# Kernel tuning notes

Measured on AMD Instinct MI355X. Metric: run time of the kernel, lower is better.

## Reference

```python
import jax, jax.numpy as jnp
import numpy as np

B, N, H, HID, MLP = 512, 96, 8, 256, 256
NODE_DIM, EDGE_DIM, E = 32, 7, 196608
DH = HID // H
NEG = -1e9  # stand-in for -inf to keep softmax NaN-free under fp16/bf16


def setup_inputs() -> dict:
    key = jax.random.key(0)
    ks = jax.random.split(key, 24)
    node_features = jax.random.normal(ks[0], (B * N, NODE_DIM), dtype=jnp.float32)
    node_batch = jnp.repeat(jnp.arange(B), N)  # sorted, exactly N nodes per graph
    g = jax.random.randint(ks[1], (E,), 0, B)
    s = jax.random.randint(ks[2], (E,), 0, N)
    d = jax.random.randint(ks[3], (E,), 0, N)
    edge_index = jnp.stack([g * N + s, g * N + d])  # [2, E] global node ids
    edge_attr = jax.random.uniform(ks[4], (E, EDGE_DIM), dtype=jnp.float32)
    def w(k, shape):
        fan_in = shape[0]
        return jax.random.normal(k, shape, dtype=jnp.float32) / np.sqrt(fan_in)
    return {
        "node_features": node_features,
        "edge_attr": edge_attr,
        "W_in1": w(ks[5], (NODE_DIM, MLP)), "b_in1": jnp.zeros((MLP,)),
        "W_in2": w(ks[6], (MLP, HID)), "b_in2": jnp.zeros((HID,)),
        "W_bond": w(ks[7], (EDGE_DIM, H)), "b_bond": jnp.zeros((H,)),
        "Wq": w(ks[8], (HID, HID)), "Wk": w(ks[9], (HID, HID)),
        "Wv": w(ks[10], (HID, HID)), "Wo": w(ks[11], (HID, HID)),
        "W_out1": w(ks[12], (HID, MLP)), "b_out1": jnp.zeros((MLP,)),
        "W_out2": w(ks[13], (MLP, 1)), "b_out2": jnp.zeros((1,)),
        "edge_index": edge_index,
        "node_batch": node_batch,
    }


def reference(node_features, edge_attr, W_in1, b_in1, W_in2, b_in2, W_bond, b_bond,
              Wq, Wk, Wv, Wo, W_out1, b_out1, W_out2, b_out2, edge_index, node_batch):
    # input MLP
    h = jax.nn.relu(node_features @ W_in1 + b_in1) @ W_in2 + b_in2  # [T, HID]
    T = h.shape[0]
    # per-graph node counts and offsets (to_dense_batch)
    counts = jax.ops.segment_sum(jnp.ones((T,), jnp.int32), node_batch, num_segments=B)
    offsets = jnp.concatenate([jnp.zeros((1,), jnp.int32), jnp.cumsum(counts)[:-1]])
    local = jnp.arange(T) - offsets[node_batch]
    dense_h = jnp.zeros((B, N, HID), h.dtype).at[node_batch, local].set(h)
    pad_mask = jnp.arange(N)[None, :] < counts[:, None]  # [B, N]
    # scatter edge features into dense bond bias + adjacency
    src, dst = edge_index
    eb = node_batch[src]
    ls = src - offsets[eb]
    ld = dst - offsets[node_batch[dst]]
    bias_flat = edge_attr @ W_bond + b_bond  # [E, H]
    bond_bias = jnp.zeros((B, N, N, H), bias_flat.dtype).at[eb, ls, ld].set(bias_flat)
    bond_bias = jnp.transpose(bond_bias, (0, 3, 1, 2))  # [B, H, N, N]
    adj = jnp.zeros((B, N, N), bool).at[eb, ls, ld].set(True)
    adj = adj | jnp.eye(N, dtype=bool)[None]  # self-loops so softmax rows are valid
    combined = jnp.where(adj[:, None], bond_bias, NEG)
    combined = jnp.where(pad_mask[:, None, None, :], combined, NEG)
    # masked multi-head attention (ESA)
    q = (dense_h @ Wq).reshape(B, N, H, DH)
    k = (dense_h @ Wk).reshape(B, N, H, DH)
    v = (dense_h @ Wv).reshape(B, N, H, DH)
    scores = jnp.einsum('bqhd,bkhd->bhqk', q, k) / np.sqrt(DH) + combined
    attn = jax.nn.softmax(scores, axis=-1)
    ctx = jnp.einsum('bhqk,bkhd->bqhd', attn, v).reshape(B, N, HID) @ Wo
    # masked mean pooling over valid nodes -> [B, HID]
    pooled = jnp.sum(ctx * pad_mask[..., None], axis=1) / counts[:, None].astype(ctx.dtype)
    logits = jax.nn.relu(pooled @ W_out1 + b_out1) @ W_out2 + b_out2
    return logits.reshape(-1)  # [B]
```

## Files before the change

kernel.cpp:

```cpp
#include <hip/hip_runtime.h>
#include <hip/hip_bf16.h>
#include <hip/hip_fp16.h>

#define BG   512
#define NN   96
#define NH   8
#define HIDD 256
#define DHD  32
#define NDIM 32
#define EDIM 7
#define NE   196608
#define TT   (BG*NN)
#define CELLS (BG*NN*NN)
#define NEGF (-60000.0f)

typedef short bf16x8 __attribute__((ext_vector_type(8)));
typedef float f32x4  __attribute__((ext_vector_type(4)));

#define MFMA16 __builtin_amdgcn_mfma_f32_16x16x32_bf16

__device__ __forceinline__ short f2bf(float x) {
    __hip_bfloat16 b = __float2bfloat16(x);
    return *reinterpret_cast<short*>(&b);
}
__device__ __forceinline__ float h2f(unsigned short u) {
    __half h = __ushort_as_half(u);
    return __half2float(h);
}

__global__ void init_winner_kernel(int* __restrict__ winner) {
    int idx = blockIdx.x * 256 + threadIdx.x;
    ((int4*)winner)[idx] = make_int4(-1, -1, -1, -1);
}

__global__ void scatter_kernel(const int* __restrict__ ei, int* __restrict__ winner) {
    int e = blockIdx.x * 256 + threadIdx.x;
    if (e >= NE) return;
    int src = ei[e], dst = ei[NE + e];
    int b  = src / NN;
    int ls = src - b * NN;
    int ld = dst % NN;
    atomicMax(&winner[b * NN * NN + ls * NN + ld], e);
}

__global__ void init_bias8_kernel(unsigned short* __restrict__ b8) {
    int idx = blockIdx.x * 256 + threadIdx.x;
    int within = idx % 1152;
    int i = within / 12, j0 = (within % 12) * 8;
    unsigned short negh = __half_as_ushort(__float2half(NEGF));
    unsigned short vals[8];
#pragma unroll
    for (int c = 0; c < 8; ++c) vals[c] = (j0 + c == i) ? (unsigned short)0 : negh;
    *(int4*)(b8 + (size_t)idx * 8) = *(int4*)vals;
}

__global__ void scatter_bias8_kernel(const int* __restrict__ ei,
                                     const int* __restrict__ winner,
                                     const float* __restrict__ ea,
                                     const float* __restrict__ Wb,
                                     const float* __restrict__ bb,
                                     unsigned short* __restrict__ b8) {
    int e = blockIdx.x * 256 + threadIdx.x;
    if (e >= NE) return;
    int src = ei[e], dst = ei[NE + e];
    int b  = src / NN;
    int ls = src - b * NN;
    int ld = dst % NN;
    int cell = b * NN * NN + ls * NN + ld;
    if (winner[cell] != e) return;
    float a[EDIM];
#pragma unroll
    for (int j = 0; j < EDIM; ++j) a[j] = ea[(size_t)e * EDIM + j];
#pragma unroll
    for (int hh = 0; hh < NH; ++hh) {
        float acc = bb[hh];
#pragma unroll
        for (int j = 0; j < EDIM; ++j) acc += a[j] * Wb[j * NH + hh];
        b8[(size_t)hh * CELLS + cell] = __half_as_ushort(__float2half(acc));
    }
}

__global__ void convert_w_kernel(const float* __restrict__ W_in2,
                                 const float* __restrict__ Wq,
                                 const float* __restrict__ Wk,
                                 const float* __restrict__ Wv,
                                 const float* __restrict__ W1,
                                 short* __restrict__ wt) {
    int m = blockIdx.x >> 8;
    int k = blockIdx.x & 255;
    if (m == 4) {
        if (k >= NDIM) return;
        wt[((size_t)(4 * HIDD) + threadIdx.x) * HIDD + k] = f2bf(W1[(size_t)k * HIDD + threadIdx.x]);
        return;
    }
    const float* W = (m == 0) ? W_in2 : (m == 1) ? Wq : (m == 2) ? Wk : Wv;
    float v = W[(size_t)k * HIDD + threadIdx.x];
    wt[((size_t)m * HIDD + threadIdx.x) * HIDD + k] = f2bf(v);
}

__global__ __launch_bounds__(256) void mlp_fused_mfma(const float* __restrict__ X,
                                                      const short* __restrict__ wt,
                                                      const float* __restrict__ b1,
                                                      const float* __restrict__ b2,
                                                      short* __restrict__ hbf) {
    __shared__ short As[64][264];
    __shared__ short Ws[256][40];
    int tid = threadIdx.x;
    int row0 = blockIdx.x * 64;
    int w = tid >> 6, l = tid & 63, lr = l & 15, g = l >> 4;
    {
        const float* xrow = X + (size_t)(row0 + w * 16 + lr) * NDIM + g * 8;
        float4 x0 = *(const float4*)xrow;
        float4 x1 = *(const float4*)(xrow + 4);
        bf16x8 af;
        af[0] = f2bf(x0.x); af[1] = f2bf(x0.y); af[2] = f2bf(x0.z); af[3] = f2bf(x0.w);
        af[4] = f2bf(x1.x); af[5] = f2bf(x1.y); af[6] = f2bf(x1.z); af[7] = f2bf(x1.w);
        const short* w1t = wt + (size_t)4 * HIDD * HIDD;
#pragma unroll
        for (int ct = 0; ct < 16; ++ct) {
            bf16x8 bfr = *(const bf16x8*)(w1t + (size_t)(ct * 16 + lr) * HIDD + g * 8);
            f32x4 acc = (f32x4){0.f, 0.f, 0.f, 0.f};
            acc = MFMA16(af, bfr, acc, 0, 0, 0);
            float bb = b1[ct * 16 + lr];
#pragma unroll
            for (int r = 0; r < 4; ++r)
                As[w * 16 + 4 * g + r][ct * 16 + lr] = f2bf(fmaxf(acc[r] + bb, 0.f));
        }
    }
    f32x4 acc[16];
#pragma unroll
    for (int ct = 0; ct < 16; ++ct) acc[ct] = (f32x4){0.f, 0.f, 0.f, 0.f};
    for (int kt = 0; kt < 8; ++kt) {
        __syncthreads();
#pragma unroll
        for (int c = 0; c < 4; ++c) {
            int q = tid + c * 256;
            int n = q >> 2, kc = (q & 3) * 8;
            *(bf16x8*)&Ws[n][kc] = *(const bf16x8*)(wt + (size_t)n * HIDD + kt * 32 + kc);
        }
        __syncthreads();
        bf16x8 af = *(const bf16x8*)&As[w * 16 + lr][kt * 32 + g * 8];
#pragma unroll
        for (int ct = 0; ct < 16; ++ct) {
            bf16x8 bfr = *(const bf16x8*)&Ws[ct * 16 + lr][g * 8];
            acc[ct] = MFMA16(af, bfr, acc[ct], 0, 0, 0);
        }
    }
#pragma unroll
    for (int ct = 0; ct < 16; ++ct) {
        int col = ct * 16 + lr;
        float bb = b2[col];
#pragma unroll
        for (int r = 0; r < 4; ++r) {
            int row = row0 + w * 16 + 4 * g + r;
            hbf[(size_t)row * HIDD + col] = f2bf(acc[ct][r] + bb);
        }
    }
}

#define WSTRIDE 264
#define WSLAB   (32 * WSTRIDE)
__global__ __launch_bounds__(384, 3) void attn_mfma_kernel(const short* __restrict__ hbf,
                                                           const short* __restrict__ wt,
                                                           const unsigned short* __restrict__ b8,
                                                           float* __restrict__ pooled) {
    __shared__ short WL[3 * WSLAB];
    __shared__ float red[24][32];
    short* Qs  = WL;
    short* Ks  = WL + 3840;
    short* Ps  = WL;
    short* VtL = WL + 22016;
    int bid = blockIdx.x;
    int b = (bid & 7) + 8 * (bid >> 6);
    int hh = (bid >> 3) & 7;
    int tid = threadIdx.x;
    int w = tid >> 6;
    int l = tid & 63, lr = l & 15, g = l >> 4;
#pragma unroll
    for (int it = 0; it < 8; ++it) {
        int c = it * 384 + tid;
        int m = c >> 10, cc = c & 1023;
        int n = cc >> 5, kc = (cc & 31) * 8;
        bf16x8 v = *(const bf16x8*)(wt + ((size_t)((1 + m) * HIDD + hh * DHD + n)) * HIDD + kc);
        *(bf16x8*)&WL[m * WSLAB + n * WSTRIDE + kc] = v;
    }
    const unsigned short* bp = b8 + (size_t)hh * CELLS + b * NN * NN;
    unsigned short bv16[6][4];
#pragma unroll
    for (int jt = 0; jt < 6; ++jt)
#pragma unroll
        for (int r = 0; r < 4; ++r)
            bv16[jt][r] = bp[(w * 16 + 4 * g + r) * NN + jt * 16 + lr];
    const short* hrow = hbf + ((size_t)(b * NN + w * 16 + lr)) * HIDD + g * 8;
    bf16x8 a[8];
#pragma unroll
    for (int ks = 0; ks < 8; ++ks) a[ks] = *(const bf16x8*)(hrow + ks * 32);
    __syncthreads();
    f32x4 qac[2], kac[2], vac[2];
#pragma unroll
    for (int ct = 0; ct < 2; ++ct) {
        qac[ct] = (f32x4){0.f, 0.f, 0.f, 0.f};
        kac[ct] = (f32x4){0.f, 0.f, 0.f, 0.f};
        vac[ct] = (f32x4){0.f, 0.f, 0.f, 0.f};
        int nrow = (ct * 16 + lr) * WSTRIDE + g * 8;
#pragma unroll
        for (int ks = 0; ks < 8; ++ks) {
            qac[ct] = MFMA16(a[ks], *(const bf16x8*)&WL[nrow + ks * 32], qac[ct], 0, 0, 0);
            kac[ct] = MFMA16(a[ks], *(const bf16x8*)&WL[WSLAB + nrow + ks * 32], kac[ct], 0, 0, 0);
            vac[ct] = MFMA16(a[ks], *(const bf16x8*)&WL[2 * WSLAB + nrow + ks * 32], vac[ct], 0, 0, 0);
        }
    }
    __syncthreads();
#pragma unroll
    for (int ct = 0; ct < 2; ++ct)
#pragma unroll
        for (int r = 0; r < 4; ++r) {
            int row = w * 16 + 4 * g + r, col = ct * 16 + lr;
            Qs[row * 40 + col]   = f2bf(qac[ct][r]);
            Ks[row * 40 + col]   = f2bf(kac[ct][r]);
            VtL[col * 104 + row] = f2bf(vac[ct][r]);
        }
    __syncthreads();
    float sc[6][4];
    {
        bf16x8 qa = *(const bf16x8*)&Qs[(w * 16 + lr) * 40 + g * 8];
        const float scale = 0.17677669529663687f;
#pragma unroll
        for (int jt = 0; jt < 6; ++jt) {
            bf16x8 kb = *(const bf16x8*)&Ks[(jt * 16 + lr) * 40 + g * 8];
            f32x4 z = (f32x4){0.f, 0.f, 0.f, 0.f};
            f32x4 s = MFMA16(qa, kb, z, 0, 0, 0);
#pragma unroll
            for (int r = 0; r < 4; ++r)
                sc[jt][r] = s[r] * scale + h2f(bv16[jt][r]);
        }
    }
#pragma unroll
    for (int r = 0; r < 4; ++r) {
        float m = sc[0][r];
#pragma unroll
        for (int jt = 1; jt < 6; ++jt) m = fmaxf(m, sc[jt][r]);
        m = fmaxf(m, __shfl_xor(m, 1)); m = fmaxf(m, __shfl_xor(m, 2));
        m = fmaxf(m, __shfl_xor(m, 4)); m = fmaxf(m, __shfl_xor(m, 8));
        float sum = 0.f;
#pragma unroll
        for (int jt = 0; jt < 6; ++jt) { sc[jt][r] = __expf(sc[jt][r] - m); sum += sc[jt][r]; }
        sum += __shfl_xor(sum, 1); sum += __shfl_xor(sum, 2);
        sum += __shfl_xor(sum, 4); sum += __shfl_xor(sum, 8);
        float inv = 1.f / sum;
#pragma unroll
        for (int jt = 0; jt < 6; ++jt) sc[jt][r] *= inv;
    }
    __syncthreads();
#pragma unroll
    for (int r = 0; r < 4; ++r) {
        int i = w * 16 + 4 * g + r;
#pragma unroll
        for (int jt = 0; jt < 6; ++jt)
            Ps[i * 104 + jt * 16 + lr] = f2bf(sc[jt][r]);
    }
    f32x4 c0 = (f32x4){0.f, 0.f, 0.f, 0.f}, c1 = (f32x4){0.f, 0.f, 0.f, 0.f};
#pragma unroll
    for (int kt = 0; kt < 3; ++kt) {
        bf16x8 pa = *(const bf16x8*)&Ps[(w * 16 + lr) * 104 + kt * 32 + g * 8];
        c0 = MFMA16(pa, *(const bf16x8*)&VtL[lr * 104 + kt * 32 + g * 8], c0, 0, 0, 0);
        c1 = MFMA16(pa, *(const bf16x8*)&VtL[(16 + lr) * 104 + kt * 32 + g * 8], c1, 0, 0, 0);
    }
    red[w * 4 + g][lr]      = c0[0] + c0[1] + c0[2] + c0[3];
    red[w * 4 + g][16 + lr] = c1[0] + c1[1] + c1[2] + c1[3];
    __syncthreads();
    if (tid < DHD) {
        float sum = 0.f;
#pragma unroll
        for (int q = 0; q < 24; ++q) sum += red[q][tid];
        pooled[(size_t)b * HIDD + hh * DHD + tid] = sum * (1.f / 96.f);
    }
}

__global__ __launch_bounds__(256) void head_kernel(const float* __restrict__ pooled,
                                                   const float* __restrict__ Wo,
                                                   const float* __restrict__ Wo1,
                                                   const float* __restrict__ bo1,
                                                   const float* __restrict__ Wo2,
                                                   const float* __restrict__ bo2,
                                                   float* __restrict__ out) {
    __shared__ float ps[HIDD];
    __shared__ float ys[HIDD];
    __shared__ float red[4];
    int b = blockIdx.x, tid = threadIdx.x;
    ps[tid] = pooled[(size_t)b * HIDD + tid];
    __syncthreads();
    float acc = 0.f;
    for (int c = 0; c < HIDD; ++c) acc += ps[c] * Wo[c * HIDD + tid];
    ys[tid] = acc;
    __syncthreads();
    float a2 = bo1[tid];
    for (int c = 0; c < HIDD; ++c) a2 += ys[c] * Wo1[c * HIDD + tid];
    float hv = fmaxf(a2, 0.f);
    float p = hv * Wo2[tid];
#pragma unroll
    for (int off = 32; off > 0; off >>= 1) p += __shfl_xor(p, off);
    int lane = tid & 63, wave = tid >> 6;
    if (lane == 0) red[wave] = p;
    __syncthreads();
    if (tid == 0) out[b] = red[0] + red[1] + red[2] + red[3] + bo2[0];
}

extern "C" void kernel_launch(void* const* d_in, const int* in_sizes, int n_in,
                              void* d_out, int out_size, void* d_ws, size_t ws_size,
                              hipStream_t stream) {
    (void)in_sizes; (void)n_in; (void)out_size;
    const float* node_features = (const float*)d_in[0];
    const float* edge_attr     = (const float*)d_in[1];
    const float* W_in1  = (const float*)d_in[2];
    const float* b_in1  = (const float*)d_in[3];
    const float* W_in2  = (const float*)d_in[4];
    const float* b_in2  = (const float*)d_in[5];
    const float* W_bond = (const float*)d_in[6];
    const float* b_bond = (const float*)d_in[7];
    const float* Wq     = (const float*)d_in[8];
    const float* Wk     = (const float*)d_in[9];
    const float* Wv     = (const float*)d_in[10];
    const float* Wo     = (const float*)d_in[11];
    const float* W_out1 = (const float*)d_in[12];
    const float* b_out1 = (const float*)d_in[13];
    const float* W_out2 = (const float*)d_in[14];
    const float* b_out2 = (const float*)d_in[15];
    const int* edge_index = (const int*)d_in[16];
    float* out = (float*)d_out;

    char* ws = (char*)d_ws;
    size_t off = 0;
    auto alloc = [&](size_t bytes) {
        void* p = ws + off;
        off = (off + bytes + 255) & ~(size_t)255;
        return p;
    };
    short*          hbf    = (short*)alloc((size_t)TT * HIDD * 2);
    short*          wt     = (short*)alloc((size_t)5 * HIDD * HIDD * 2);
    unsigned short* b8     = (unsigned short*)alloc((size_t)NH * CELLS * 2);
    int*            winner = (int*)alloc((size_t)CELLS * 4);
    float*          pooled = (float*)alloc((size_t)BG * HIDD * 4);
    if (ws_size < off) return;

    hipLaunchKernelGGL(init_winner_kernel, dim3(CELLS / 1024), dim3(256), 0, stream, winner);
    hipLaunchKernelGGL(scatter_kernel, dim3((NE + 255) / 256), dim3(256), 0, stream, edge_index, winner);
    hipLaunchKernelGGL(init_bias8_kernel, dim3(NH * CELLS / 8 / 256), dim3(256), 0, stream, b8);
    hipLaunchKernelGGL(scatter_bias8_kernel, dim3((NE + 255) / 256), dim3(256), 0, stream,
                       edge_index, winner, edge_attr, W_bond, b_bond, b8);
    hipLaunchKernelGGL(convert_w_kernel, dim3(5 * 256), dim3(256), 0, stream,
                       W_in2, Wq, Wk, Wv, W_in1, wt);
    hipLaunchKernelGGL(mlp_fused_mfma, dim3(TT / 64), dim3(256), 0, stream,
                       node_features, wt, b_in1, b_in2, hbf);
    hipLaunchKernelGGL(attn_mfma_kernel, dim3(BG * NH), dim3(384), 0, stream,
                       hbf, wt, b8, pooled);
    hipLaunchKernelGGL(head_kernel, dim3(BG), dim3(256), 0, stream,
                       pooled, Wo, W_out1, b_out1, W_out2, b_out2, out);
}
```

Measured before the change: 248.5 us.

## Process two graphs per attention block with pre-swizzled QKV weight fragments

The attention kernel now handles two graphs per block for the same head, so each block loads the per-head Q/K/V weight slab once and reuses it for both graphs. The weights are pre-arranged into MFMA fragment order in a new workspace buffer, which lets the kernel copy them into shared memory with flat loads and no padding. The three setup kernels (winner init, bias init, weight convert) are merged into one launch. In exchange, register pressure rises and occupancy drops (launch bounds go from 3 to 2 blocks), and the grid is half as large.

```diff
diff --git a/kernel.cpp b/kernel.cpp
--- a/kernel.cpp
+++ b/kernel.cpp
@@ -28,9 +28,62 @@
     return __half2float(h);
 }
 
-__global__ void init_winner_kernel(int* __restrict__ winner) {
-    int idx = blockIdx.x * 256 + threadIdx.x;
-    ((int4*)winner)[idx] = make_int4(-1, -1, -1, -1);
+#define JA 4608
+#define JB 18432
+#define JC 512
+#define JD 96
+__global__ void setup_kernel(int* __restrict__ winner,
+                             unsigned short* __restrict__ b8,
+                             short* __restrict__ wt,
+                             short* __restrict__ wf,
+                             const float* __restrict__ W_in2,
+                             const float* __restrict__ W1,
+                             const float* __restrict__ Wq,
+                             const float* __restrict__ Wk,
+                             const float* __restrict__ Wv) {
+    int blk = blockIdx.x, tid = threadIdx.x;
+    if (blk < JA) {
+        ((int4*)winner)[blk * 256 + tid] = make_int4(-1, -1, -1, -1);
+        return;
+    }
+    blk -= JA;
+    if (blk < JB) {
+        int idx = blk * 256 + tid;
+        int within = idx % 1152;
+        int i = within / 12, j0 = (within % 12) * 8;
+        unsigned short negh = __half_as_ushort(__float2half(NEGF));
+        unsigned short vals[8];
+#pragma unroll
+        for (int c = 0; c < 8; ++c) vals[c] = (j0 + c == i) ? (unsigned short)0 : negh;
+        *(int4*)(b8 + (size_t)idx * 8) = *(int4*)vals;
+        return;
+    }
+    blk -= JB;
+    if (blk < JC) {
+        int mm = blk >> 8, k = blk & 255;
+        if (mm == 1) {
+            if (k < NDIM)
+                wt[((size_t)(4 * HIDD) + tid) * HIDD + k] = f2bf(W1[(size_t)k * HIDD + tid]);
+        } else {
+            wt[(size_t)tid * HIDD + k] = f2bf(W_in2[(size_t)k * HIDD + tid]);
+        }
+        return;
+    }
+    blk -= JC;
+    {
+        int gi = blk * 4 + (tid >> 6);
+        int lane = tid & 63, lr = lane & 15, gg = lane >> 4;
+        int ks = gi & 7, ct = (gi >> 3) & 1, hh = (gi >> 4) & 7, m = gi >> 7;
+        const float* W = (m == 0) ? Wq : (m == 1) ? Wk : Wv;
+        int col = hh * DHD + ct * 16 + lr;
+        short v[8];
+#pragma unroll
+        for (int e = 0; e < 8; ++e) {
+            int k = ks * 32 + gg * 8 + e;
+            v[e] = f2bf(W[(size_t)k * HIDD + col]);
+        }
+        *(bf16x8*)(wf + ((size_t)gi * 64 + lane) * 8) = *(bf16x8*)v;
+    }
 }
 
 __global__ void scatter_kernel(const int* __restrict__ ei, int* __restrict__ winner) {
@@ -41,17 +94,6 @@
     int ls = src - b * NN;
     int ld = dst % NN;
     atomicMax(&winner[b * NN * NN + ls * NN + ld], e);
-}
-
-__global__ void init_bias8_kernel(unsigned short* __restrict__ b8) {
-    int idx = blockIdx.x * 256 + threadIdx.x;
-    int within = idx % 1152;
-    int i = within / 12, j0 = (within % 12) * 8;
-    unsigned short negh = __half_as_ushort(__float2half(NEGF));
-    unsigned short vals[8];
-#pragma unroll
-    for (int c = 0; c < 8; ++c) vals[c] = (j0 + c == i) ? (unsigned short)0 : negh;
-    *(int4*)(b8 + (size_t)idx * 8) = *(int4*)vals;
 }
 
 __global__ void scatter_bias8_kernel(const int* __restrict__ ei,
@@ -78,24 +120,6 @@
         for (int j = 0; j < EDIM; ++j) acc += a[j] * Wb[j * NH + hh];
         b8[(size_t)hh * CELLS + cell] = __half_as_ushort(__float2half(acc));
     }
-}
-
-__global__ void convert_w_kernel(const float* __restrict__ W_in2,
-                                 const float* __restrict__ Wq,
-                                 const float* __restrict__ Wk,
-                                 const float* __restrict__ Wv,
-                                 const float* __restrict__ W1,
-                                 short* __restrict__ wt) {
-    int m = blockIdx.x >> 8;
-    int k = blockIdx.x & 255;
-    if (m == 4) {
-        if (k >= NDIM) return;
-        wt[((size_t)(4 * HIDD) + threadIdx.x) * HIDD + k] = f2bf(W1[(size_t)k * HIDD + threadIdx.x]);
-        return;
-    }
-    const float* W = (m == 0) ? W_in2 : (m == 1) ? Wq : (m == 2) ? Wk : Wv;
-    float v = W[(size_t)k * HIDD + threadIdx.x];
-    wt[((size_t)m * HIDD + threadIdx.x) * HIDD + k] = f2bf(v);
 }
 
 __global__ __launch_bounds__(256) void mlp_fused_mfma(const float* __restrict__ X,
@@ -158,21 +182,19 @@
     }
 }
 
-#define WSTRIDE 264
-#define WSLAB   (32 * WSTRIDE)
-__global__ __launch_bounds__(384, 3) void attn_mfma_kernel(const short* __restrict__ hbf,
-                                                           const short* __restrict__ wt,
-                                                           const unsigned short* __restrict__ b8,
-                                                           float* __restrict__ pooled) {
-    __shared__ short WL[3 * WSLAB];
-    __shared__ float red[24][32];
-    short* Qs  = WL;
-    short* Ks  = WL + 3840;
-    short* Ps  = WL;
-    short* VtL = WL + 22016;
+__global__ __launch_bounds__(384, 2) void attn2_kernel(const short* __restrict__ hbf,
+                                                       const short* __restrict__ wf,
+                                                       const unsigned short* __restrict__ b8,
+                                                       float* __restrict__ pooled) {
+    __shared__ short WL[24576];
+    __shared__ float red2[2][24][32];
+    short* Qs2 = WL;
+    short* Ks2 = WL + 7680;
+    short* Ps2 = WL;
+    short* Vt2 = WL + 18432;
     int bid = blockIdx.x;
-    int b = (bid & 7) + 8 * (bid >> 6);
-    int hh = (bid >> 3) & 7;
+    int g8 = bid & 7, hh = (bid >> 3) & 7, pr = bid >> 6;
+    int b0 = g8 + 16 * pr, b1 = b0 + 8;
     int tid = threadIdx.x;
     int w = tid >> 6;
     int l = tid & 63, lr = l & 15, g = l >> 4;
@@ -180,34 +202,43 @@
     for (int it = 0; it < 8; ++it) {
         int c = it * 384 + tid;
         int m = c >> 10, cc = c & 1023;
-        int n = cc >> 5, kc = (cc & 31) * 8;
-        bf16x8 v = *(const bf16x8*)(wt + ((size_t)((1 + m) * HIDD + hh * DHD + n)) * HIDD + kc);
-        *(bf16x8*)&WL[m * WSLAB + n * WSTRIDE + kc] = v;
-    }
-    const unsigned short* bp = b8 + (size_t)hh * CELLS + b * NN * NN;
-    unsigned short bv16[6][4];
-#pragma unroll
-    for (int jt = 0; jt < 6; ++jt)
-#pragma unroll
-        for (int r = 0; r < 4; ++r)
-            bv16[jt][r] = bp[(w * 16 + 4 * g + r) * NN + jt * 16 + lr];
-    const short* hrow = hbf + ((size_t)(b * NN + w * 16 + lr)) * HIDD + g * 8;
-    bf16x8 a[8];
-#pragma unroll
-    for (int ks = 0; ks < 8; ++ks) a[ks] = *(const bf16x8*)(hrow + ks * 32);
-    __syncthreads();
-    f32x4 qac[2], kac[2], vac[2];
+        *(bf16x8*)&WL[m * 8192 + cc * 8] =
+            *(const bf16x8*)(wf + (((size_t)(m * 8 + hh)) * 1024 + cc) * 8);
+    }
+    unsigned short bv16[2][6][4];
+#pragma unroll
+    for (int gr = 0; gr < 2; ++gr) {
+        const unsigned short* bp = b8 + (size_t)hh * CELLS + (size_t)(gr ? b1 : b0) * NN * NN;
+#pragma unroll
+        for (int jt = 0; jt < 6; ++jt)
+#pragma unroll
+            for (int r = 0; r < 4; ++r)
+                bv16[gr][jt][r] = bp[(w * 16 + 4 * g + r) * NN + jt * 16 + lr];
+    }
+    const short* h0 = hbf + ((size_t)(b0 * NN + w * 16 + lr)) * HIDD + g * 8;
+    const short* h1 = hbf + ((size_t)(b1 * NN + w * 16 + lr)) * HIDD + g * 8;
+    bf16x8 a0[8], a1[8];
+#pragma unroll
+    for (int ks = 0; ks < 8; ++ks) { a0[ks] = *(const bf16x8*)(h0 + ks * 32);
+                                     a1[ks] = *(const bf16x8*)(h1 + ks * 32); }
+    __syncthreads();
+    f32x4 q0[2], k0[2], v0[2], q1[2], k1[2], v1[2];
 #pragma unroll
     for (int ct = 0; ct < 2; ++ct) {
-        qac[ct] = (f32x4){0.f, 0.f, 0.f, 0.f};
-        kac[ct] = (f32x4){0.f, 0.f, 0.f, 0.f};
-        vac[ct] = (f32x4){0.f, 0.f, 0.f, 0.f};
-        int nrow = (ct * 16 + lr) * WSTRIDE + g * 8;
+        q0[ct] = (f32x4){0.f,0.f,0.f,0.f}; k0[ct] = q0[ct]; v0[ct] = q0[ct];
+        q1[ct] = q0[ct]; k1[ct] = q0[ct]; v1[ct] = q0[ct];
 #pragma unroll
         for (int ks = 0; ks < 8; ++ks) {
-            qac[ct] = MFMA16(a[ks], *(const bf16x8*)&WL[nrow + ks * 32], qac[ct], 0, 0, 0);
-            kac[ct] = MFMA16(a[ks], *(const bf16x8*)&WL[WSLAB + nrow + ks * 32], kac[ct], 0, 0, 0);
-            vac[ct] = MFMA16(a[ks], *(const bf16x8*)&WL[2 * WSLAB + nrow + ks * 32], vac[ct], 0, 0, 0);
+            int fo = ((ct * 8 + ks) * 64 + l) * 8;
+            bf16x8 bq = *(const bf16x8*)&WL[fo];
+            bf16x8 bk = *(const bf16x8*)&WL[8192 + fo];
+            bf16x8 bv = *(const bf16x8*)&WL[16384 + fo];
+            q0[ct] = MFMA16(a0[ks], bq, q0[ct], 0, 0, 0);
+            q1[ct] = MFMA16(a1[ks], bq, q1[ct], 0, 0, 0);
+            k0[ct] = MFMA16(a0[ks], bk, k0[ct], 0, 0, 0);
+            k1[ct] = MFMA16(a1[ks], bk, k1[ct], 0, 0, 0);
+            v0[ct] = MFMA16(a0[ks], bv, v0[ct], 0, 0, 0);
+            v1[ct] = MFMA16(a1[ks], bv, v1[ct], 0, 0, 0);
         }
     }
     __syncthreads();
@@ -216,64 +247,74 @@
 #pragma unroll
         for (int r = 0; r < 4; ++r) {
             int row = w * 16 + 4 * g + r, col = ct * 16 + lr;
-            Qs[row * 40 + col]   = f2bf(qac[ct][r]);
-            Ks[row * 40 + col]   = f2bf(kac[ct][r]);
-            VtL[col * 104 + row] = f2bf(vac[ct][r]);
-        }
-    __syncthreads();
-    float sc[6][4];
-    {
-        bf16x8 qa = *(const bf16x8*)&Qs[(w * 16 + lr) * 40 + g * 8];
-        const float scale = 0.17677669529663687f;
+            Qs2[row * 40 + col]          = f2bf(q0[ct][r]);
+            Qs2[3840 + row * 40 + col]   = f2bf(q1[ct][r]);
+            Ks2[row * 40 + col]          = f2bf(k0[ct][r]);
+            Ks2[3840 + row * 40 + col]   = f2bf(k1[ct][r]);
+            Vt2[col * 96 + row]          = f2bf(v0[ct][r]);
+            Vt2[3072 + col * 96 + row]   = f2bf(v1[ct][r]);
+        }
+    __syncthreads();
+    float sc2[2][6][4];
+    const float scale = 0.17677669529663687f;
+#pragma unroll
+    for (int gr = 0; gr < 2; ++gr) {
+        bf16x8 qa = *(const bf16x8*)&Qs2[gr * 3840 + (w * 16 + lr) * 40 + g * 8];
 #pragma unroll
         for (int jt = 0; jt < 6; ++jt) {
-            bf16x8 kb = *(const bf16x8*)&Ks[(jt * 16 + lr) * 40 + g * 8];
+            bf16x8 kb = *(const bf16x8*)&Ks2[gr * 3840 + (jt * 16 + lr) * 40 + g * 8];
             f32x4 z = (f32x4){0.f, 0.f, 0.f, 0.f};
             f32x4 s = MFMA16(qa, kb, z, 0, 0, 0);
 #pragma unroll
             for (int r = 0; r < 4; ++r)
-                sc[jt][r] = s[r] * scale + h2f(bv16[jt][r]);
-        }
-    }
-#pragma unroll
-    for (int r = 0; r < 4; ++r) {
-        float m = sc[0][r];
-#pragma unroll
-        for (int jt = 1; jt < 6; ++jt) m = fmaxf(m, sc[jt][r]);
-        m = fmaxf(m, __shfl_xor(m, 1)); m = fmaxf(m, __shfl_xor(m, 2));
-        m = fmaxf(m, __shfl_xor(m, 4)); m = fmaxf(m, __shfl_xor(m, 8));
+                sc2[gr][jt][r] = s[r] * scale + h2f(bv16[gr][jt][r]);
+        }
+#pragma unroll
+        for (int r = 0; r < 4; ++r) {
+            float m = sc2[gr][0][r];
+#pragma unroll
+            for (int jt = 1; jt < 6; ++jt) m = fmaxf(m, sc2[gr][jt][r]);
+            m = fmaxf(m, __shfl_xor(m, 1)); m = fmaxf(m, __shfl_xor(m, 2));
+            m = fmaxf(m, __shfl_xor(m, 4)); m = fmaxf(m, __shfl_xor(m, 8));
+            float sum = 0.f;
+#pragma unroll
+            for (int jt = 0; jt < 6; ++jt) { sc2[gr][jt][r] = __expf(sc2[gr][jt][r] - m); sum += sc2[gr][jt][r]; }
+            sum += __shfl_xor(sum, 1); sum += __shfl_xor(sum, 2);
+            sum += __shfl_xor(sum, 4); sum += __shfl_xor(sum, 8);
+            float inv = 1.f / sum;
+#pragma unroll
+            for (int jt = 0; jt < 6; ++jt) sc2[gr][jt][r] *= inv;
+        }
+    }
+    __syncthreads();
+#pragma unroll
+    for (int gr = 0; gr < 2; ++gr)
+#pragma unroll
+        for (int r = 0; r < 4; ++r) {
+            int i = w * 16 + 4 * g + r;
+#pragma unroll
+            for (int jt = 0; jt < 6; ++jt)
+                Ps2[gr * 9216 + i * 96 + jt * 16 + lr] = f2bf(sc2[gr][jt][r]);
+        }
+#pragma unroll
+    for (int gr = 0; gr < 2; ++gr) {
+        f32x4 c0 = (f32x4){0.f,0.f,0.f,0.f}, c1 = (f32x4){0.f,0.f,0.f,0.f};
+#pragma unroll
+        for (int kt = 0; kt < 3; ++kt) {
+            bf16x8 pa = *(const bf16x8*)&Ps2[gr * 9216 + (w * 16 + lr) * 96 + kt * 32 + g * 8];
+            c0 = MFMA16(pa, *(const bf16x8*)&Vt2[gr * 3072 + lr * 96 + kt * 32 + g * 8], c0, 0, 0, 0);
+            c1 = MFMA16(pa, *(const bf16x8*)&Vt2[gr * 3072 + (16 + lr) * 96 + kt * 32 + g * 8], c1, 0, 0, 0);
+        }
+        red2[gr][w * 4 + g][lr]      = c0[0] + c0[1] + c0[2] + c0[3];
+        red2[gr][w * 4 + g][16 + lr] = c1[0] + c1[1] + c1[2] + c1[3];
+    }
+    __syncthreads();
+    if (tid < 64) {
+        int gr = tid >> 5, d = tid & 31;
         float sum = 0.f;
 #pragma unroll
-        for (int jt = 0; jt < 6; ++jt) { sc[jt][r] = __expf(sc[jt][r] - m); sum += sc[jt][r]; }
-        sum += __shfl_xor(sum, 1); sum += __shfl_xor(sum, 2);
-        sum += __shfl_xor(sum, 4); sum += __shfl_xor(sum, 8);
-        float inv = 1.f / sum;
-#pragma unroll
-        for (int jt = 0; jt < 6; ++jt) sc[jt][r] *= inv;
-    }
-    __syncthreads();
-#pragma unroll
-    for (int r = 0; r < 4; ++r) {
-        int i = w * 16 + 4 * g + r;
-#pragma unroll
-        for (int jt = 0; jt < 6; ++jt)
-            Ps[i * 104 + jt * 16 + lr] = f2bf(sc[jt][r]);
-    }
-    f32x4 c0 = (f32x4){0.f, 0.f, 0.f, 0.f}, c1 = (f32x4){0.f, 0.f, 0.f, 0.f};
-#pragma unroll
-    for (int kt = 0; kt < 3; ++kt) {
-        bf16x8 pa = *(const bf16x8*)&Ps[(w * 16 + lr) * 104 + kt * 32 + g * 8];
-        c0 = MFMA16(pa, *(const bf16x8*)&VtL[lr * 104 + kt * 32 + g * 8], c0, 0, 0, 0);
-        c1 = MFMA16(pa, *(const bf16x8*)&VtL[(16 + lr) * 104 + kt * 32 + g * 8], c1, 0, 0, 0);
-    }
-    red[w * 4 + g][lr]      = c0[0] + c0[1] + c0[2] + c0[3];
-    red[w * 4 + g][16 + lr] = c1[0] + c1[1] + c1[2] + c1[3];
-    __syncthreads();
-    if (tid < DHD) {
-        float sum = 0.f;
-#pragma unroll
-        for (int q = 0; q < 24; ++q) sum += red[q][tid];
-        pooled[(size_t)b * HIDD + hh * DHD + tid] = sum * (1.f / 96.f);
+        for (int q = 0; q < 24; ++q) sum += red2[gr][q][d];
+        pooled[(size_t)(gr ? b1 : b0) * HIDD + hh * DHD + d] = sum * (1.f / 96.f);
     }
 }
 
@@ -338,22 +379,22 @@
     };
     short*          hbf    = (short*)alloc((size_t)TT * HIDD * 2);
     short*          wt     = (short*)alloc((size_t)5 * HIDD * HIDD * 2);
+    short*          wf     = (short*)alloc((size_t)384 * 64 * 8 * 2);
     unsigned short* b8     = (unsigned short*)alloc((size_t)NH * CELLS * 2);
     int*            winner = (int*)alloc((size_t)CELLS * 4);
     float*          pooled = (float*)alloc((size_t)BG * HIDD * 4);
     if (ws_size < off) return;
 
-    hipLaunchKernelGGL(init_winner_kernel, dim3(CELLS / 1024), dim3(256), 0, stream, winner);
-    hipLaunchKernelGGL(scatter_kernel, dim3((NE + 255) / 256), dim3(256), 0, stream, edge_index, winner);
-    hipLaunchKernelGGL(init_bias8_kernel, dim3(NH * CELLS / 8 / 256), dim3(256), 0, stream, b8);
+    hipLaunchKernelGGL(setup_kernel, dim3(JA + JB + JC + JD), dim3(256), 0, stream,
+                       winner, b8, wt, wf, W_in2, W_in1, Wq, Wk, Wv);
+    hipLaunchKernelGGL(scatter_kernel, dim3((NE + 255) / 256), dim3(256), 0, stream,
+                       edge_index, winner);
     hipLaunchKernelGGL(scatter_bias8_kernel, dim3((NE + 255) / 256), dim3(256), 0, stream,
                        edge_index, winner, edge_attr, W_bond, b_bond, b8);
-    hipLaunchKernelGGL(convert_w_kernel, dim3(5 * 256), dim3(256), 0, stream,
-                       W_in2, Wq, Wk, Wv, W_in1, wt);
     hipLaunchKernelGGL(mlp_fused_mfma, dim3(TT / 64), dim3(256), 0, stream,
                        node_features, wt, b_in1, b_in2, hbf);
-    hipLaunchKernelGGL(attn_mfma_kernel, dim3(BG * NH), dim3(384), 0, stream,
-                       hbf, wt, b8, pooled);
+    hipLaunchKernelGGL(attn2_kernel, dim3(BG * NH / 2), dim3(384), 0, stream,
+                       hbf, wf, b8, pooled);
     hipLaunchKernelGGL(head_kernel, dim3(BG), dim3(256), 0, stream,
                        pooled, Wo, W_out1, b_out1, W_out2, b_out2, out);
 }
```

After: 258.5 us. 1.04x slower.
